# Optimization experiments

Measured on AMD Instinct MI355X. Metric: run time of the kernel, lower is better.

Reference implementation:

```python
import jax, jax.numpy as jnp
import numpy as np
from jax.scipy.linalg import solve_triangular

B, D, NL, NH, DH = 16, 768, 12, 12, 64
P, S, LP, NC = 10, 5, 5, 100
IMG, PATCH = 224, 16
NPTOK = (IMG // PATCH) ** 2  # 196 patches
DFF = 4 * D
LOG2PI = float(np.log(2.0 * np.pi))


def setup_inputs() -> dict:
    key = jax.random.key(0)
    ks = jax.random.split(key, 12)
    s = 0.02
    inp = {}
    inp['inputs'] = jax.random.normal(ks[0], (B, 3, IMG, IMG), jnp.float32)
    inp['patch_w'] = jax.random.normal(ks[1], (D, 3, PATCH, PATCH), jnp.float32) * s
    inp['patch_b'] = jnp.zeros((D,), jnp.float32)
    inp['cls_token'] = jax.random.normal(ks[2], (1, 1, D), jnp.float32) * s
    inp['pos_embed'] = jax.random.normal(ks[3], (1, NPTOK + 1, D), jnp.float32) * s
    inp['ln1_g'] = jnp.ones((NL, D), jnp.float32)
    inp['ln1_b'] = jnp.zeros((NL, D), jnp.float32)
    inp['qkv_w'] = jax.random.normal(ks[4], (NL, D, 3 * D), jnp.float32) * s
    inp['qkv_b'] = jnp.zeros((NL, 3 * D), jnp.float32)
    inp['proj_w'] = jax.random.normal(ks[5], (NL, D, D), jnp.float32) * s
    inp['proj_b'] = jnp.zeros((NL, D), jnp.float32)
    inp['ln2_g'] = jnp.ones((NL, D), jnp.float32)
    inp['ln2_b'] = jnp.zeros((NL, D), jnp.float32)
    inp['fc1_w'] = jax.random.normal(ks[6], (NL, D, DFF), jnp.float32) * s
    inp['fc1_b'] = jnp.zeros((NL, DFF), jnp.float32)
    inp['fc2_w'] = jax.random.normal(ks[7], (NL, DFF, D), jnp.float32) * s
    inp['fc2_b'] = jnp.zeros((NL, D), jnp.float32)
    inp['norm_g'] = jnp.ones((D,), jnp.float32)
    inp['norm_b'] = jnp.zeros((D,), jnp.float32)
    inp['head_w'] = jax.random.normal(ks[8], (D, NC), jnp.float32) * s
    inp['head_b'] = jnp.zeros((NC,), jnp.float32)
    inp['prompt'] = jax.random.normal(ks[9], (P, LP, D), jnp.float32)
    m = jax.random.normal(ks[10], (P, D), jnp.float32)
    inp['mean'] = m / jnp.linalg.norm(m, axis=-1, keepdims=True)
    # init in torch: ones + eye, repeated per pool component (positive definite)
    inp['variance'] = jnp.ones((P, D, D), jnp.float32) + jnp.eye(D, dtype=jnp.float32)[None]
    return inp


def _ln(x, g, b, eps=1e-6):
    m = x.mean(-1, keepdims=True)
    v = jnp.mean((x - m) ** 2, axis=-1, keepdims=True)
    return (x - m) * jax.lax.rsqrt(v + eps) * g + b


def _blocks(x, blk):
    def step(x, pl):
        g1, b1, qw, qb, pw, pb, g2, b2, f1w, f1b, f2w, f2b = pl
        Bn, N, _ = x.shape
        h = _ln(x, g1, b1)
        qkv = (h @ qw + qb).reshape(Bn, N, 3, NH, DH).transpose(2, 0, 3, 1, 4)
        q, k, v = qkv[0], qkv[1], qkv[2]  # [B,H,N,dh]
        att = jax.nn.softmax(jnp.einsum('bhqd,bhkd->bhqk', q, k) * (1.0 / np.sqrt(DH)), axis=-1)
        o = jnp.einsum('bhqk,bhkd->bhqd', att, v).transpose(0, 2, 1, 3).reshape(Bn, N, D)
        x = x + o @ pw + pb
        h = _ln(x, g2, b2)
        return x + jax.nn.gelu(h @ f1w + f1b) @ f2w + f2b, None
    x, _ = jax.lax.scan(step, x, blk)
    return x


def _mvn_logprob(q, mean, cov):
    # q: [B,D]; mean: [P,D]; cov: [P,D,D] -> [B,P]
    L = jnp.linalg.cholesky(cov)
    diff = q[:, None, :] - mean[None]  # [B,P,D]
    y = jax.vmap(lambda Lp, dp: solve_triangular(Lp, dp.T, lower=True), in_axes=(0, 1))(L, diff)  # [P,D,B]
    quad = jnp.sum(y * y, axis=1).T  # [B,P]
    logdet = 2.0 * jnp.sum(jnp.log(jnp.diagonal(L, axis1=-2, axis2=-1)), axis=-1)  # [P]
    return -0.5 * (D * LOG2PI + logdet[None, :] + quad)


def reference(inputs, patch_w, patch_b, cls_token, pos_embed, ln1_g, ln1_b, qkv_w, qkv_b,
              proj_w, proj_b, ln2_g, ln2_b, fc1_w, fc1_b, fc2_w, fc2_b, norm_g, norm_b,
              head_w, head_b, prompt, mean, variance):
    blk = (ln1_g, ln1_b, qkv_w, qkv_b, proj_w, proj_b, ln2_g, ln2_b, fc1_w, fc1_b, fc2_w, fc2_b)
    # patch embed: conv16x16 stride16 -> [B,196,D]
    img = jax.lax.conv_general_dilated(inputs, patch_w, (PATCH, PATCH), 'VALID',
                                       dimension_numbers=('NCHW', 'OIHW', 'NCHW'))
    img = img.reshape(B, D, NPTOK).transpose(0, 2, 1) + patch_b
    t = jnp.concatenate([jnp.broadcast_to(cls_token, (B, 1, D)), img], axis=1)
    x0 = t + pos_embed
    # query pass (no_grad in original)
    q = _ln(_blocks(x0, blk), norm_g, norm_b)[:, 0]  # [B,D]
    cov = jnp.abs(variance) + jnp.eye(D, dtype=variance.dtype)[None]
    logp = _mvn_logprob(q, mean, cov)  # [B,P]
    _, topk = jax.lax.top_k(logp, S)  # [B,S]
    prompts = prompt[topk].reshape(B, S * LP, D) + pos_embed[0, 0]
    # prompted pass: [cls(+pos), prompts, raw patch tokens]
    x = jnp.concatenate([x0[:, :1], prompts, img], axis=1)  # [B, 1+S*LP+196, D]
    x = _ln(_blocks(x, blk), norm_g, norm_b)
    x = x[:, 1:S * LP + 1].mean(axis=1)  # mean over prompt tokens
    return x @ head_w + head_b  # [B,NC]
```

## Files before the change

kernel.cpp:

```cpp
#include <hip/hip_runtime.h>
#include <stdint.h>
#include <math.h>


typedef _Float16 h16_t;
typedef _Float16 h8v __attribute__((ext_vector_type(8)));
typedef _Float16 h4v __attribute__((ext_vector_type(4)));
typedef float    f4v __attribute__((ext_vector_type(4)));

#define DEV static __device__ __forceinline__

DEV float wred64(float s) {
#pragma unroll
  for (int m = 1; m < 64; m <<= 1) s += __shfl_xor(s, m, 64);
  return s;
}
DEV float gelu_f(float x) {
  float u = 0.7978845608028654f * x * (1.0f + 0.044715f * x * x);
  u = fminf(fmaxf(u, -30.0f), 30.0f);
  float e = __expf(-2.0f * u);
  return 0.5f * x * (1.0f + (1.0f - e) / (1.0f + e));
}

#define GLD16(gp, lp) __builtin_amdgcn_global_load_lds( \
  (const __attribute__((address_space(1))) unsigned int*)(const void*)(gp), \
  (__attribute__((address_space(3))) unsigned int*)(void*)(lp), 16, 0, 0)

template <int R>
DEV void stgN(const h16_t* __restrict__ src, int row0, int rowmax, int ldk,
              char* ldsb, unsigned lbase, int tid) {
#pragma unroll
  for (int r = 0; r < R; r++) {
    unsigned P = ((unsigned)r << 13) + ((unsigned)tid << 4);
    unsigned Q = P ^ (((P >> 7) & 3u) << 4);
    int row = (int)(Q >> 6);
    int kb = (int)((Q & 63u) >> 1);
    int gr = row0 + row; gr = gr < rowmax ? gr : rowmax - 1;
    GLD16(src + (size_t)gr * ldk + kb,
          ldsb + lbase + (r << 13) + ((tid >> 6) << 10));
  }
}

#define FENCE() asm volatile("" ::: "memory")
#define RBAR() do { FENCE(); __builtin_amdgcn_s_barrier(); FENCE(); } while (0)
#define VMW(N) asm volatile("s_waitcnt vmcnt(" #N ")" ::: "memory")

DEV h8v frag_rd(const char* ldsb, unsigned rb, int row, int quad) {
  unsigned P = ((unsigned)row << 6) + ((unsigned)quad << 4);
  P ^= ((P >> 7) & 3u) << 4;
  return *(const h8v*)(ldsb + rb + P);
}

__global__ __launch_bounds__(512, 2) void hgemm_q(
    const h16_t* __restrict__ A, const h16_t* __restrict__ B,
    h16_t* __restrict__ C16, const float* __restrict__ bias,
    int M, int N, int K, int ldc16)
{
  __shared__ __align__(16) char ldsb[147456];
  int tid = threadIdx.x;
  int w = tid >> 6, lane = tid & 63;
  int wm = w >> 2, wn = w & 3;
  int fr = lane & 15, quad = lane >> 4;
  int m0 = blockIdx.x << 7, n0 = blockIdx.y << 8;

  f4v acc[4][4];
#pragma unroll
  for (int i2 = 0; i2 < 4; i2++)
#pragma unroll
    for (int j2 = 0; j2 < 4; j2++)
#pragma unroll
      for (int r2 = 0; r2 < 4; r2++) acc[i2][j2][r2] = 0.0f;

  int NT = K >> 6;

  auto stage = [&](int t, unsigned bb) {
    stgN<1>(A + (t << 6),      m0, M, K, ldsb, bb,           tid);
    stgN<1>(A + (t << 6) + 32, m0, M, K, ldsb, bb + 8192u,   tid);
    stgN<2>(B + (t << 6),      n0, N, K, ldsb, bb + 16384u,  tid);
    stgN<2>(B + (t << 6) + 32, n0, N, K, ldsb, bb + 32768u,  tid);
  };
  stage(0, 0u);
  stage(1, 49152u);
  VMW(6);
  __builtin_amdgcn_s_barrier();
  FENCE();

  unsigned cb = 0u, sb = 98304u;
  for (int i = 0; i < NT; i++) {
    int tS = (i + 2 < NT) ? i + 2 : NT - 1;
    stage(tS, sb);
    h8v af[2][4], bf[2][4];
#pragma unroll
    for (int kh = 0; kh < 2; kh++)
#pragma unroll
      for (int t = 0; t < 4; t++) {
        af[kh][t] = frag_rd(ldsb, cb + ((unsigned)kh << 13),
                            (wm << 6) + (t << 4) + fr, quad);
        bf[kh][t] = frag_rd(ldsb, cb + 16384u + ((unsigned)kh << 14),
                            (wn << 6) + (t << 4) + fr, quad);
      }
    __builtin_amdgcn_s_setprio(1);
#pragma unroll
    for (int kh = 0; kh < 2; kh++)
#pragma unroll
      for (int ti = 0; ti < 4; ti++)
#pragma unroll
        for (int tj = 0; tj < 4; tj++)
          acc[ti][tj] = __builtin_amdgcn_mfma_f32_16x16x32_f16(af[kh][ti], bf[kh][tj], acc[ti][tj], 0, 0, 0);
    __builtin_amdgcn_s_setprio(0);
    VMW(6);
    RBAR();
    cb = (cb == 98304u) ? 0u : cb + 49152u;
    sb = (sb == 98304u) ? 0u : sb + 49152u;
  }
  asm volatile("s_waitcnt vmcnt(0)" ::: "memory");

  int row0 = m0 + (wm << 6) + (quad << 2);
  int col0 = n0 + (wn << 6) + fr;
  float bv[4];
#pragma unroll
  for (int nj = 0; nj < 4; nj++) bv[nj] = bias[col0 + (nj << 4)];
#pragma unroll
  for (int mi = 0; mi < 4; mi++) {
#pragma unroll
    for (int rg = 0; rg < 4; rg++) {
      int row = row0 + (mi << 4) + rg;
      if (row < M) {
#pragma unroll
        for (int nj = 0; nj < 4; nj++) {
          float v = acc[mi][nj][rg] + bv[nj];
          C16[(size_t)row * ldc16 + col0 + (nj << 4)] = (h16_t)v;
        }
      }
    }
  }
}

__global__ __launch_bounds__(512, 2) void hgemm_f(
    const h16_t* __restrict__ A, const h16_t* __restrict__ B,
    h16_t* __restrict__ C16, const float* __restrict__ bias,
    int M, int N, int K, int ldc16)
{
  __shared__ __align__(16) char ldsb[98304];
  int tid = threadIdx.x;
  int w = tid >> 6, lane = tid & 63;
  int wm = w >> 2, wn = w & 3;
  int fr = lane & 15, quad = lane >> 4;
  int m0 = blockIdx.x << 8, n0 = blockIdx.y << 8;

  f4v acc[8][4];
#pragma unroll
  for (int i2 = 0; i2 < 8; i2++)
#pragma unroll
    for (int j2 = 0; j2 < 4; j2++)
#pragma unroll
      for (int r2 = 0; r2 < 4; r2++) acc[i2][j2][r2] = 0.0f;

  int NT = K >> 5;

  auto stage = [&](int t, unsigned bb) {
    stgN<2>(A + (t << 5), m0, M, K, ldsb, bb,          tid);
    stgN<2>(B + (t << 5), n0, N, K, ldsb, bb + 16384u, tid);
  };
  stage(0, 0u);
  stage(1, 32768u);
  VMW(4);
  __builtin_amdgcn_s_barrier();
  FENCE();

  unsigned cb = 0u, sb = 65536u;
  for (int i = 0; i < NT; i++) {
    int tS = (i + 2 < NT) ? i + 2 : NT - 1;
    stage(tS, sb);
    h8v af[8], bf[4];
#pragma unroll
    for (int t = 0; t < 8; t++)
      af[t] = frag_rd(ldsb, cb, (wm << 7) + (t << 4) + fr, quad);
#pragma unroll
    for (int t = 0; t < 4; t++)
      bf[t] = frag_rd(ldsb, cb + 16384u, (wn << 6) + (t << 4) + fr, quad);
    __builtin_amdgcn_s_setprio(1);
#pragma unroll
    for (int ti = 0; ti < 8; ti++)
#pragma unroll
      for (int tj = 0; tj < 4; tj++)
        acc[ti][tj] = __builtin_amdgcn_mfma_f32_16x16x32_f16(af[ti], bf[tj], acc[ti][tj], 0, 0, 0);
    __builtin_amdgcn_s_setprio(0);
    VMW(4);
    RBAR();
    cb = (cb == 65536u) ? 0u : cb + 32768u;
    sb = (sb == 65536u) ? 0u : sb + 32768u;
  }
  asm volatile("s_waitcnt vmcnt(0)" ::: "memory");

  int row0 = m0 + (wm << 7) + (quad << 2);
  int col0 = n0 + (wn << 6) + fr;
  float bv[4];
#pragma unroll
  for (int nj = 0; nj < 4; nj++) bv[nj] = bias[col0 + (nj << 4)];
#pragma unroll
  for (int mi = 0; mi < 8; mi++) {
#pragma unroll
    for (int rg = 0; rg < 4; rg++) {
      int row = row0 + (mi << 4) + rg;
      if (row < M) {
#pragma unroll
        for (int nj = 0; nj < 4; nj++) {
          float v = gelu_f(acc[mi][nj][rg] + bv[nj]);
          C16[(size_t)row * ldc16 + col0 + (nj << 4)] = (h16_t)v;
        }
      }
    }
  }
}

__global__ __launch_bounds__(512, 2) void hgemm_p(
    const h16_t* __restrict__ A, const h16_t* __restrict__ B,
    float* __restrict__ C32, const float* __restrict__ bias,
    int M, int N, int K, int ldc, int addC)
{
  __shared__ __align__(16) char ldsb[98304];
  int tid = threadIdx.x;
  int w = tid >> 6, lane = tid & 63;
  int wm = w >> 2, wn = w & 3;
  int fr = lane & 15, quad = lane >> 4;
  int m0 = blockIdx.x << 7, n0 = blockIdx.y << 7;

  f4v acc[4][2];
#pragma unroll
  for (int i2 = 0; i2 < 4; i2++)
#pragma unroll
    for (int j2 = 0; j2 < 2; j2++)
#pragma unroll
      for (int r2 = 0; r2 < 4; r2++) acc[i2][j2][r2] = 0.0f;

  int NT = K >> 6;

  auto stage = [&](int t, unsigned bb) {
    stgN<1>(A + (t << 6),      m0, M, K, ldsb, bb,           tid);
    stgN<1>(A + (t << 6) + 32, m0, M, K, ldsb, bb + 8192u,   tid);
    stgN<1>(B + (t << 6),      n0, N, K, ldsb, bb + 16384u,  tid);
    stgN<1>(B + (t << 6) + 32, n0, N, K, ldsb, bb + 24576u,  tid);
  };
  stage(0, 0u);
  stage(1, 32768u);
  VMW(4);
  __builtin_amdgcn_s_barrier();
  FENCE();

  unsigned cb = 0u, sb = 65536u;
  for (int i = 0; i < NT; i++) {
    int tS = (i + 2 < NT) ? i + 2 : NT - 1;
    stage(tS, sb);
    h8v af[2][4], bf[2][2];
#pragma unroll
    for (int kh = 0; kh < 2; kh++) {
#pragma unroll
      for (int t = 0; t < 4; t++)
        af[kh][t] = frag_rd(ldsb, cb + ((unsigned)kh << 13),
                            (wm << 6) + (t << 4) + fr, quad);
#pragma unroll
      for (int t = 0; t < 2; t++)
        bf[kh][t] = frag_rd(ldsb, cb + 16384u + ((unsigned)kh << 13),
                            (wn << 5) + (t << 4) + fr, quad);
    }
    __builtin_amdgcn_s_setprio(1);
#pragma unroll
    for (int kh = 0; kh < 2; kh++)
#pragma unroll
      for (int ti = 0; ti < 4; ti++)
#pragma unroll
        for (int tj = 0; tj < 2; tj++)
          acc[ti][tj] = __builtin_amdgcn_mfma_f32_16x16x32_f16(af[kh][ti], bf[kh][tj], acc[ti][tj], 0, 0, 0);
    __builtin_amdgcn_s_setprio(0);
    VMW(4);
    RBAR();
    cb = (cb == 65536u) ? 0u : cb + 32768u;
    sb = (sb == 65536u) ? 0u : sb + 32768u;
  }
  asm volatile("s_waitcnt vmcnt(0)" ::: "memory");

  int row0 = m0 + (wm << 6) + (quad << 2);
  int col0 = n0 + (wn << 5) + fr;
  float bv[2];
#pragma unroll
  for (int nj = 0; nj < 2; nj++) bv[nj] = bias[col0 + (nj << 4)];
#pragma unroll
  for (int mi = 0; mi < 4; mi++) {
#pragma unroll
    for (int rg = 0; rg < 4; rg++) {
      int row = row0 + (mi << 4) + rg;
      if (row < M) {
#pragma unroll
        for (int nj = 0; nj < 2; nj++) {
          size_t off = (size_t)row * ldc + col0 + (nj << 4);
          float v = acc[mi][nj][rg] + bv[nj];
          if (addC) v += C32[off];
          C32[off] = v;
        }
      }
    }
  }
}

__global__ __launch_bounds__(256) void flash_attn(
    const h16_t* __restrict__ qkv, h16_t* __restrict__ o, int N)
{
  int z = blockIdx.y;
  int b = z / 12, h = z - (z / 12) * 12;
  const h16_t* base = qkv + (size_t)b * N * 2304 + h * 64;
  int q0 = blockIdx.x << 6;
  int tid = threadIdx.x, w = tid >> 6, lane = tid & 63;
  int fr = lane & 15, fk = (lane >> 4) << 3;
  int quad = lane >> 4;

  __shared__ __align__(16) h16_t Qs[2][64 * 32];
  __shared__ __align__(16) h16_t Ks[2][64 * 32];
  __shared__ __align__(16) h16_t Ps[4][1024];
  __shared__ __align__(16) h16_t Vt[64 * 68];

#pragma unroll
  for (int s = 0; s < 2; s++) {
    int gq = q0 + (w << 4) + (lane >> 2); gq = gq < N ? gq : N - 1;
    GLD16(base + (size_t)gq * 2304 + (s << 5) + ((lane & 3) << 3), &Qs[s][(w << 4) << 5]);
  }
  __syncthreads();
  h8v af0 = *(const h8v*)&Qs[0][(((w << 4) + fr) << 5) + fk];
  h8v af1 = *(const h8v*)&Qs[1][(((w << 4) + fr) << 5) + fk];

  float mrow[4], lrow[4];
  f4v accO[4];
#pragma unroll
  for (int r = 0; r < 4; r++) { mrow[r] = -1e30f; lrow[r] = 0.0f; }
#pragma unroll
  for (int t = 0; t < 4; t++)
#pragma unroll
    for (int r = 0; r < 4; r++) accO[t][r] = 0.0f;

  int nj = (N + 63) >> 6;
  for (int jt = 0; jt < nj; jt++) {
    int j0 = jt << 6;
    __syncthreads();
#pragma unroll
    for (int s = 0; s < 2; s++) {
      int gj = j0 + (w << 4) + (lane >> 2); gj = gj < N ? gj : N - 1;
      GLD16(base + (size_t)gj * 2304 + 768 + (s << 5) + ((lane & 3) << 3), &Ks[s][(w << 4) << 5]);
    }
#pragma unroll
    for (int i = 0; i < 16; i++) {
      int j = (w << 4) + i;
      int gj = j0 + j; gj = gj < N ? gj : N - 1;
      Vt[lane * 68 + j] = base[(size_t)gj * 2304 + 1536 + lane];
    }
    __syncthreads();

    f4v s4[4];
#pragma unroll
    for (int t = 0; t < 4; t++) {
      h8v b0 = *(const h8v*)&Ks[0][(((t << 4) + fr) << 5) + fk];
      h8v b1 = *(const h8v*)&Ks[1][(((t << 4) + fr) << 5) + fk];
      f4v s; s[0] = s[1] = s[2] = s[3] = 0.0f;
      s = __builtin_amdgcn_mfma_f32_16x16x32_f16(af0, b0, s, 0, 0, 0);
      s = __builtin_amdgcn_mfma_f32_16x16x32_f16(af1, b1, s, 0, 0, 0);
      s4[t] = s;
    }
#pragma unroll
    for (int r = 0; r < 4; r++) {
      float tm = -1e30f;
#pragma unroll
      for (int t = 0; t < 4; t++) {
        float v = s4[t][r] * 0.125f;
        if (j0 + (t << 4) + fr >= N) v = -1e30f;
        s4[t][r] = v;
        tm = fmaxf(tm, v);
      }
#pragma unroll
      for (int m = 1; m < 16; m <<= 1) tm = fmaxf(tm, __shfl_xor(tm, m, 64));
      float mn = fmaxf(mrow[r], tm);
      float alpha = __expf(mrow[r] - mn);
      mrow[r] = mn;
      float rs = 0.0f;
#pragma unroll
      for (int t = 0; t < 4; t++) {
        float e = __expf(s4[t][r] - mn);
        s4[t][r] = e;
        rs += e;
      }
#pragma unroll
      for (int m = 1; m < 16; m <<= 1) rs += __shfl_xor(rs, m, 64);
      lrow[r] = lrow[r] * alpha + rs;
#pragma unroll
      for (int t = 0; t < 4; t++) accO[t][r] *= alpha;
#pragma unroll
      for (int t = 0; t < 4; t++)
        Ps[w][((t >> 1) << 9) + (((quad << 2) + r) << 5) + ((t & 1) << 4) + fr] = (h16_t)s4[t][r];
    }
#pragma unroll
    for (int s = 0; s < 2; s++) {
      h8v ap = *(const h8v*)&Ps[w][(s << 9) + (fr << 5) + fk];
#pragma unroll
      for (int t = 0; t < 4; t++) {
        int vidx = ((t << 4) + fr) * 68 + (s << 5) + fk;
        h4v v0 = *(const h4v*)&Vt[vidx];
        h4v v1 = *(const h4v*)&Vt[vidx + 4];
        h8v bv;
#pragma unroll
        for (int i = 0; i < 4; i++) { bv[i] = v0[i]; bv[i + 4] = v1[i]; }
        accO[t] = __builtin_amdgcn_mfma_f32_16x16x32_f16(ap, bv, accO[t], 0, 0, 0);
      }
    }
  }

#pragma unroll
  for (int r = 0; r < 4; r++) {
    int q = q0 + (w << 4) + (quad << 2) + r;
    if (q >= N) continue;
    float inv = 1.0f / lrow[r];
    h16_t* op = o + ((size_t)b * N + q) * 768 + h * 64 + fr;
#pragma unroll
    for (int t = 0; t < 4; t++) op[t << 4] = (h16_t)(accO[t][r] * inv);
  }
}

__global__ __launch_bounds__(256) void wcvt_t(const float* __restrict__ in,
                                              h16_t* __restrict__ o, int K, int N) {
  int z = blockIdx.z;
  in += (size_t)z * K * N;
  o  += (size_t)z * K * N;
  int n0 = blockIdx.x << 5, k0 = blockIdx.y << 5;
  __shared__ float t[32][33];
  int a = threadIdx.x >> 3, b4 = (threadIdx.x & 7) << 2;
  f4v v = *(const f4v*)(in + (size_t)(k0 + a) * N + n0 + b4);
  t[a][b4] = v[0]; t[a][b4 + 1] = v[1]; t[a][b4 + 2] = v[2]; t[a][b4 + 3] = v[3];
  __syncthreads();
  h4v h;
#pragma unroll
  for (int i = 0; i < 4; i++) h[i] = (h16_t)t[b4 + i][a];
  *(h4v*)(o + (size_t)(n0 + a) * K + k0 + b4) = h;
}

__global__ void cvt_flat(const float* __restrict__ in, h16_t* __restrict__ o, int n) {
  int i = blockIdx.x * 256 + threadIdx.x;
  if (i < n) o[i] = (h16_t)in[i];
}

__global__ void im2col_k(const float* __restrict__ in, h16_t* __restrict__ col) {
  int idx = blockIdx.x * 256 + threadIdx.x;
  if (idx >= 16 * 196 * 768) return;
  int k = idx % 768; int t = idx / 768; int p2 = t % 196; int b = t / 196;
  int c = k >> 8, ij = k & 255, i = ij >> 4, j = ij & 15;
  int py = p2 / 14, px = p2 % 14;
  col[idx] = (h16_t)in[(((size_t)b * 3 + c) * 224 + py * 16 + i) * 224 + px * 16 + j];
}

__global__ void build_x0_k(float* __restrict__ x, const float* __restrict__ img,
                           const float* __restrict__ cls, const float* __restrict__ pos) {
  int idx = blockIdx.x * 256 + threadIdx.x;
  if (idx >= 16 * 197 * 768) return;
  int d = idx % 768; int t = idx / 768; int n = t % 197; int b = t / 197;
  float v = (n == 0) ? cls[d] : img[((size_t)b * 196 + (n - 1)) * 768 + d];
  x[idx] = v + pos[n * 768 + d];
}

__global__ void build_x2_k(float* __restrict__ x, const float* __restrict__ img,
                           const float* __restrict__ cls, const float* __restrict__ pos,
                           const float* __restrict__ prompt, const int* __restrict__ tk) {
  int idx = blockIdx.x * 256 + threadIdx.x;
  if (idx >= 16 * 222 * 768) return;
  int d = idx % 768; int t = idx / 768; int n = t % 222; int b = t / 222;
  float v;
  if (n == 0) v = cls[d] + pos[d];
  else if (n < 26) {
    int s = (n - 1) / 5, li = (n - 1) % 5;
    v = prompt[((size_t)tk[b * 5 + s] * 5 + li) * 768 + d] + pos[d];
  } else {
    v = img[((size_t)b * 196 + (n - 26)) * 768 + d];
  }
  x[idx] = v;
}

__global__ void ln_rows(const float* __restrict__ in, h16_t* __restrict__ o16,
                        float* __restrict__ o32, const float* __restrict__ g,
                        const float* __restrict__ b, int rows, long istr, long ostr) {
  int gw = ((blockIdx.x << 8) + threadIdx.x) >> 6;
  int lane = threadIdx.x & 63;
  if (gw >= rows) return;
  const float* rp = in + (size_t)gw * istr;
  float v[12]; float s = 0;
#pragma unroll
  for (int i = 0; i < 12; i++) { v[i] = rp[lane + (i << 6)]; s += v[i]; }
  s = wred64(s);
  float mean = s * (1.0f / 768.0f);
  float s2 = 0;
#pragma unroll
  for (int i = 0; i < 12; i++) { float d = v[i] - mean; s2 += d * d; }
  s2 = wred64(s2);
  float rstd = rsqrtf(s2 * (1.0f / 768.0f) + 1e-6f);
#pragma unroll
  for (int i = 0; i < 12; i++) {
    int k = lane + (i << 6);
    float o = (v[i] - mean) * rstd * g[k] + b[k];
    if (o16) o16[(size_t)gw * ostr + k] = (h16_t)o;
    if (o32) o32[(size_t)gw * ostr + k] = o;
  }
}

__global__ void cov_init_k(const float* __restrict__ var, float* __restrict__ Lb) {
  size_t i = (size_t)blockIdx.x * 256 + threadIdx.x;
  if (i >= (size_t)10 * 589824) return;
  int ij = (int)(i % 589824);
  int r = ij / 768, c = ij - r * 768;
  Lb[i] = fabsf(var[i]) + ((r == c) ? 1.0f : 0.0f);
}

__global__ __launch_bounds__(256) void sgemm_nt_chol(float* __restrict__ Lb, int jb) {
  int p = blockIdx.z;
  float* base = Lb + (size_t)p * 589824;
  const float* A = base + (size_t)jb * 768;
  const float* Bp = A;
  float* C = base + (size_t)jb * 768 + jb;
  int m0 = blockIdx.x << 6;
  __shared__ float As[16][64];
  __shared__ float Bs[16][64];
  int tid = threadIdx.x;
  int am = tid & 63, ak = (tid >> 6) << 2;
  int tm = (tid >> 4) << 2, tn = (tid & 15) << 2;
  float acc[4][4] = {};
  for (int k0 = 0; k0 < jb; k0 += 16) {
    f4v va = *(const f4v*)(A + (size_t)(m0 + am) * 768 + k0 + ak);
    f4v vb = *(const f4v*)(Bp + (size_t)am * 768 + k0 + ak);
#pragma unroll
    for (int i = 0; i < 4; i++) { As[ak + i][am] = va[i]; Bs[ak + i][am] = vb[i]; }
    __syncthreads();
#pragma unroll
    for (int kk = 0; kk < 16; kk++) {
      f4v a = *(const f4v*)&As[kk][tm];
      f4v b = *(const f4v*)&Bs[kk][tn];
#pragma unroll
      for (int i = 0; i < 4; i++)
#pragma unroll
        for (int j = 0; j < 4; j++) acc[i][j] += a[i] * b[j];
    }
    __syncthreads();
  }
#pragma unroll
  for (int i = 0; i < 4; i++)
#pragma unroll
    for (int j = 0; j < 4; j++)
      C[(size_t)(m0 + tm + i) * 768 + tn + j] -= acc[i][j];
}

template <int CB>
DEV void chol_sub(float (&row)[64], int r, bool actv, float* Bl, float* Dg, float* Dinv) {
  if constexpr (CB > 0) {
    if (actv && r >= CB && r < CB + 16) {
      int c = r - CB;
#pragma unroll
      for (int k = 0; k < CB; k++) Bl[k * 16 + c] = row[k];
    }
    __syncthreads();
    if (actv && r >= CB) {
#pragma unroll
      for (int k = 0; k < CB; k++) {
        float a = row[k];
#pragma unroll
        for (int c = 0; c < 16; c++) row[CB + c] -= a * Bl[k * 16 + c];
      }
    }
  }
  __syncthreads();
  if (r >= CB && r < CB + 16) {
    int c = r - CB;
#pragma unroll
    for (int j = 0; j < 16; j++) {
      float dv = __shfl(row[CB + j], CB + j, 64);
      float ds = sqrtf(dv);
      float di = 1.0f / ds;
      if (c == j) row[CB + j] = ds;
      else if (c > j) row[CB + j] *= di;
#pragma unroll
      for (int c2 = j + 1; c2 < 16; c2++) {
        float lc2 = __shfl(row[CB + j], CB + c2, 64);
        if (c >= c2) row[CB + c2] -= row[CB + j] * lc2;
      }
    }
#pragma unroll
    for (int j = 0; j < 16; j++) Dg[c * 16 + j] = row[CB + j];
    Dinv[c] = 1.0f / row[CB + c];
  }
  __syncthreads();
  if (actv && r >= CB + 16) {
#pragma unroll
    for (int c2 = 0; c2 < 16; c2++) {
      float v = row[CB + c2];
#pragma unroll
      for (int k = 0; k < c2; k++) v -= row[CB + k] * Dg[c2 * 16 + k];
      row[CB + c2] = v * Dinv[c2];
    }
  }
  __syncthreads();
}

__global__ __launch_bounds__(768) void chol_panel(float* __restrict__ Lb, int jb) {
  int p = blockIdx.x;
  float* L = Lb + (size_t)p * 589824;
  int R = 768 - jb;
  int r = threadIdx.x;
  bool actv = r < R;
  __shared__ float Bl[48 * 16];
  __shared__ float Dg[256];
  __shared__ float Dinv[16];
  float row[64];
  float* my = L + (size_t)(jb + r) * 768 + jb;
  if (actv) {
#pragma unroll
    for (int i = 0; i < 16; i++) {
      f4v v = *(const f4v*)(my + 4 * i);
      row[4 * i] = v[0]; row[4 * i + 1] = v[1]; row[4 * i + 2] = v[2]; row[4 * i + 3] = v[3];
    }
  }
  chol_sub<0>(row, r, actv, Bl, Dg, Dinv);
  chol_sub<16>(row, r, actv, Bl, Dg, Dinv);
  chol_sub<32>(row, r, actv, Bl, Dg, Dinv);
  chol_sub<48>(row, r, actv, Bl, Dg, Dinv);
  if (actv) {
#pragma unroll
    for (int i = 0; i < 16; i++) {
      f4v v; v[0] = row[4 * i]; v[1] = row[4 * i + 1]; v[2] = row[4 * i + 2]; v[3] = row[4 * i + 3];
      *(f4v*)(my + 4 * i) = v;
    }
  }
}

__global__ __launch_bounds__(256) void ltrans_k(const float* __restrict__ Lb,
                                                float* __restrict__ Ut,
                                                float* __restrict__ dg) {
  int p = blockIdx.z;
  const float* L = Lb + (size_t)p * 589824;
  float* U = Ut + (size_t)p * 589824;
  int r0 = blockIdx.x << 5, c0 = blockIdx.y << 5;
  __shared__ float t[32][33];
  int a = threadIdx.x >> 3, b4 = (threadIdx.x & 7) << 2;
  f4v v = *(const f4v*)(L + (size_t)(r0 + a) * 768 + c0 + b4);
  t[a][b4] = v[0]; t[a][b4 + 1] = v[1]; t[a][b4 + 2] = v[2]; t[a][b4 + 3] = v[3];
  __syncthreads();
  int k = c0 + a;
  f4v ov;
#pragma unroll
  for (int i = 0; i < 4; i++) {
    int j = r0 + b4 + i;
    float val = t[b4 + i][a];
    ov[i] = (j > k) ? val : 0.0f;
    if (j == k) dg[p * 768 + k] = val;
  }
  *(f4v*)(U + (size_t)k * 768 + r0 + b4) = ov;
}

__global__ __launch_bounds__(64) void trsm2(const float* __restrict__ Ut,
                                            const float* __restrict__ dg,
                                            const float* __restrict__ q,
                                            const float* __restrict__ mean,
                                            float* __restrict__ logp) {
  int gw = blockIdx.x;
  int p = gw >> 4, b = gw & 15;
  const float* U = Ut + (size_t)p * 589824;
  int lane = threadIdx.x;

  float y[12], dinv[12];
  float lacc = 0.0f;
#pragma unroll
  for (int m = 0; m < 12; m++) {
    int i = lane + (m << 6);
    y[m] = q[b * 768 + i] - mean[p * 768 + i];
    float d = dg[p * 768 + i];
    dinv[m] = 1.0f / d;
    lacc += __logf(d);
  }

  float u[8][12];
#pragma unroll
  for (int d0 = 0; d0 < 8; d0++)
#pragma unroll
    for (int mm = 0; mm < 12; mm++)
      u[d0][mm] = U[(size_t)d0 * 768 + lane + (mm << 6)];

#pragma unroll
  for (int m = 0; m < 12; m++) {
    for (int kb = 0; kb < 64; kb += 8) {
#pragma unroll
      for (int kd = 0; kd < 8; kd++) {
        int k = (m << 6) + kb + kd;
        float yo = __shfl(y[m], kb + kd, 64);
        float di = __shfl(dinv[m], kb + kd, 64);
        float yk = yo * di;
        if (lane == kb + kd) y[m] = yk;
        float un[12];
        bool pf = (k + 8) < 768;
        const float* rp = U + (size_t)(k + 8) * 768 + lane;
#pragma unroll
        for (int mm = 0; mm < 12; mm++) un[mm] = pf ? rp[mm << 6] : 0.0f;
#pragma unroll
        for (int mm = 0; mm < 12; mm++) y[mm] -= u[kd][mm] * yk;
#pragma unroll
        for (int mm = 0; mm < 12; mm++) u[kd][mm] = un[mm];
      }
    }
  }

  float quad = 0.0f;
#pragma unroll
  for (int m = 0; m < 12; m++) quad += y[m] * y[m];
  quad = wred64(quad);
  lacc = wred64(lacc);
  if (lane == 0)
    logp[b * 10 + p] = -0.5f * (768.0f * 1.8378770664093453f + 2.0f * lacc + quad);
}

__global__ void topk_k(const float* __restrict__ logp, int* __restrict__ tk) {
  int b = threadIdx.x;
  if (b >= 16) return;
  float v[10];
#pragma unroll
  for (int p = 0; p < 10; p++) v[p] = logp[b * 10 + p];
#pragma unroll
  for (int s = 0; s < 5; s++) {
    int bi = 0; float bv = v[0];
#pragma unroll
    for (int p = 1; p < 10; p++) if (v[p] > bv) { bv = v[p]; bi = p; }
    tk[b * 5 + s] = bi;
    v[bi] = -3.0e38f;
  }
}

DEV float blocksum256(float s, float* red) {
  s = wred64(s);
  __syncthreads();
  if ((threadIdx.x & 63) == 0) red[threadIdx.x >> 6] = s;
  __syncthreads();
  return red[0] + red[1] + red[2] + red[3];
}

__global__ __launch_bounds__(256) void final_head(const float* __restrict__ x,
                                                  const float* __restrict__ g,
                                                  const float* __restrict__ b,
                                                  const float* __restrict__ hw,
                                                  const float* __restrict__ hb,
                                                  float* __restrict__ out) {
  int bb = blockIdx.x, tid = threadIdx.x;
  __shared__ float xm[768];
  __shared__ float red[4];
  float a0 = 0, a1 = 0, a2 = 0;
  for (int j = 1; j <= 25; j++) {
    const float* rp = x + ((size_t)bb * 222 + j) * 768;
    float v0 = rp[tid], v1 = rp[tid + 256], v2 = rp[tid + 512];
    float s = blocksum256(v0 + v1 + v2, red);
    float mean = s * (1.0f / 768.0f);
    float d0 = v0 - mean, d1 = v1 - mean, d2 = v2 - mean;
    float s2 = blocksum256(d0 * d0 + d1 * d1 + d2 * d2, red);
    float rstd = rsqrtf(s2 * (1.0f / 768.0f) + 1e-6f);
    a0 += d0 * rstd * g[tid] + b[tid];
    a1 += d1 * rstd * g[tid + 256] + b[tid + 256];
    a2 += d2 * rstd * g[tid + 512] + b[tid + 512];
  }
  xm[tid] = a0 * (1.0f / 25.0f);
  xm[tid + 256] = a1 * (1.0f / 25.0f);
  xm[tid + 512] = a2 * (1.0f / 25.0f);
  __syncthreads();
  if (tid < 100) {
    float s = hb[tid];
    for (int d = 0; d < 768; d++) s += xm[d] * hw[d * 100 + tid];
    out[bb * 100 + tid] = s;
  }
}

extern "C" void kernel_launch(void* const* d_in, const int* in_sizes, int n_in,
                              void* d_out, int out_size, void* d_ws, size_t ws_size,
                              hipStream_t stream) {
  (void)in_sizes; (void)n_in; (void)out_size; (void)ws_size;
  const float* inp     = (const float*)d_in[0];
  const float* patchw  = (const float*)d_in[1];
  const float* patchb  = (const float*)d_in[2];
  const float* cls     = (const float*)d_in[3];
  const float* pos     = (const float*)d_in[4];
  const float* ln1g    = (const float*)d_in[5];
  const float* ln1b    = (const float*)d_in[6];
  const float* qkvw    = (const float*)d_in[7];
  const float* qkvb    = (const float*)d_in[8];
  const float* projw   = (const float*)d_in[9];
  const float* projb   = (const float*)d_in[10];
  const float* ln2g    = (const float*)d_in[11];
  const float* ln2b    = (const float*)d_in[12];
  const float* fc1w    = (const float*)d_in[13];
  const float* fc1b    = (const float*)d_in[14];
  const float* fc2w    = (const float*)d_in[15];
  const float* fc2b    = (const float*)d_in[16];
  const float* normg   = (const float*)d_in[17];
  const float* normb   = (const float*)d_in[18];
  const float* headw   = (const float*)d_in[19];
  const float* headb   = (const float*)d_in[20];
  const float* prompt  = (const float*)d_in[21];
  const float* meanp   = (const float*)d_in[22];
  const float* var     = (const float*)d_in[23];
  float* out = (float*)d_out;

  char* ws = (char*)d_ws;
  size_t cur = 0;
  auto alloc = [&](size_t bytes) { size_t r = cur; cur += (bytes + 255) & ~(size_t)255; return r; };
  float* x    = (float*)(ws + alloc((size_t)3552 * 768 * 4));
  float* img  = (float*)(ws + alloc((size_t)3136 * 768 * 4));
  float* qb   = (float*)(ws + alloc((size_t)16 * 768 * 4));
  float* logp = (float*)(ws + alloc(1024));
  int*   tk   = (int*)(ws + alloc(1024));
  float* dg   = (float*)(ws + alloc((size_t)10 * 768 * 4));
  h16_t* h16   = (h16_t*)(ws + alloc((size_t)3552 * 768 * 2));
  size_t qkv_off = alloc((size_t)3552 * 2304 * 2);
  h16_t* qkv16 = (h16_t*)(ws + qkv_off);
  size_t g_off = alloc((size_t)3552 * 3072 * 2);
  h16_t* g16   = (h16_t*)(ws + g_off);
  float* Lbuf  = (float*)(ws + alloc((size_t)10 * 589824 * 4));
  h16_t* wq16  = (h16_t*)(ws + alloc((size_t)12 * 2304 * 768 * 2));
  h16_t* wp16  = (h16_t*)(ws + alloc((size_t)12 * 768 * 768 * 2));
  h16_t* w116  = (h16_t*)(ws + alloc((size_t)12 * 3072 * 768 * 2));
  h16_t* w216  = (h16_t*)(ws + alloc((size_t)12 * 768 * 3072 * 2));
  h16_t* wpt16 = (h16_t*)(ws + alloc((size_t)768 * 768 * 2));
  h16_t* col16 = (h16_t*)(ws + g_off);
  float* Ut    = (float*)(ws + qkv_off);

  wcvt_t<<<dim3(72, 24, 12), 256, 0, stream>>>(qkvw, wq16, 768, 2304);
  wcvt_t<<<dim3(24, 24, 12), 256, 0, stream>>>(projw, wp16, 768, 768);
  wcvt_t<<<dim3(96, 24, 12), 256, 0, stream>>>(fc1w, w116, 768, 3072);
  wcvt_t<<<dim3(24, 96, 12), 256, 0, stream>>>(fc2w, w216, 3072, 768);
  cvt_flat<<<2304, 256, 0, stream>>>(patchw, wpt16, 589824);

  im2col_k<<<9408, 256, 0, stream>>>(inp, col16);
  hgemm_p<<<dim3(25, 6), 512, 0, stream>>>(col16, wpt16, img, patchb,
      3136, 768, 768, 768, 0);
  build_x0_k<<<9456, 256, 0, stream>>>(x, img, cls, pos);

  auto pass = [&](int Ntok) {
    int M = 16 * Ntok;
    int Mt1 = (M + 127) / 128;
    int Mt8 = (M + 255) / 256;
    int Qt = (Ntok + 63) / 64;
    for (int l = 0; l < 12; l++) {
      ln_rows<<<(M + 3) / 4, 256, 0, stream>>>(x, h16, nullptr, ln1g + l * 768, ln1b + l * 768, M, 768, 768);
      hgemm_q<<<dim3(Mt1, 9), 512, 0, stream>>>(h16, wq16 + (size_t)l * 2304 * 768, qkv16,
          qkvb + l * 2304, M, 2304, 768, 2304);
      flash_attn<<<dim3(Qt, 192), 256, 0, stream>>>(qkv16, h16, Ntok);
      hgemm_p<<<dim3(Mt1, 6), 512, 0, stream>>>(h16, wp16 + (size_t)l * 768 * 768, x,
          projb + l * 768, M, 768, 768, 768, 1);
      ln_rows<<<(M + 3) / 4, 256, 0, stream>>>(x, h16, nullptr, ln2g + l * 768, ln2b + l * 768, M, 768, 768);
      hgemm_f<<<dim3(Mt8, 12), 512, 0, stream>>>(h16, w116 + (size_t)l * 3072 * 768, g16,
          fc1b + l * 3072, M, 3072, 768, 3072);
      hgemm_p<<<dim3(Mt1, 6), 512, 0, stream>>>(g16, w216 + (size_t)l * 768 * 3072, x,
          fc2b + l * 768, M, 768, 3072, 768, 1);
    }
  };

  pass(197);
  ln_rows<<<4, 256, 0, stream>>>(x, nullptr, qb, normg, normb, 16, (long)197 * 768, 768);

  cov_init_k<<<23040, 256, 0, stream>>>(var, Lbuf);
  for (int m = 0; m < 12; m++) {
    int jb = 64 * m;
    if (m) sgemm_nt_chol<<<dim3((768 - jb) / 64, 1, 10), 256, 0, stream>>>(Lbuf, jb);
    chol_panel<<<10, 768, 0, stream>>>(Lbuf, jb);
  }
  ltrans_k<<<dim3(24, 24, 10), 256, 0, stream>>>(Lbuf, Ut, dg);
  trsm2<<<160, 64, 0, stream>>>(Ut, dg, qb, meanp, logp);
  topk_k<<<1, 64, 0, stream>>>(logp, tk);

  build_x2_k<<<10656, 256, 0, stream>>>(x, img, cls, pos, prompt, tk);
  pass(222);
  final_head<<<16, 256, 0, stream>>>(x, normg, normb, headw, headb, out);
}
```

Baseline: 5.333 ms.

## Switch blocked Cholesky from left-looking panel to right-looking diag/trsm/syrk steps

Replaces the left-looking blocked Cholesky (a GEMM update followed by a single 768-thread panel kernel per matrix) with a right-looking scheme. Each step factors the 64x64 diagonal block in one wave, solves the off-diagonal panel with one thread per row, and applies a lower-triangular trailing SYRK update over many 64x64 tiles. The aim is more parallel blocks per step than the old 10-block panel kernel, which did serial sub-block work. In exchange there are more kernel launches, the trailing submatrix is re-read and re-written at every step, and the diagonal factorization runs in only 64 threads per matrix.

```diff
diff --git a/kernel.cpp b/kernel.cpp
--- a/kernel.cpp
+++ b/kernel.cpp
@@ -513,21 +513,93 @@
   Lb[i] = fabsf(var[i]) + ((r == c) ? 1.0f : 0.0f);
 }
 
-__global__ __launch_bounds__(256) void sgemm_nt_chol(float* __restrict__ Lb, int jb) {
+__global__ __launch_bounds__(64) void chol_diag(float* __restrict__ Lb, int jb) {
+  int p = blockIdx.x;
+  float* base = Lb + (size_t)p * 589824 + (size_t)jb * 768 + jb;
+  int r = threadIdx.x;
+  float* rp = base + (size_t)r * 768;
+  float a[64];
+#pragma unroll
+  for (int i = 0; i < 16; i++) {
+    f4v v = *(const f4v*)(rp + 4 * i);
+    a[4 * i] = v[0]; a[4 * i + 1] = v[1]; a[4 * i + 2] = v[2]; a[4 * i + 3] = v[3];
+  }
+#pragma unroll
+  for (int j = 0; j < 64; j++) {
+    float dv = __shfl(a[j], j, 64);
+    float ds = sqrtf(dv);
+    float di = 1.0f / ds;
+    if (r == j) a[j] = ds;
+    else if (r > j) a[j] *= di;
+    float lrj = a[j];
+#pragma unroll
+    for (int c = j + 1; c < 64; c++) {
+      float lcj = __shfl(a[j], c, 64);
+      if (r >= c) a[c] -= lrj * lcj;
+    }
+  }
+#pragma unroll
+  for (int i = 0; i < 16; i++) {
+    f4v v;
+    v[0] = a[4 * i]; v[1] = a[4 * i + 1]; v[2] = a[4 * i + 2]; v[3] = a[4 * i + 3];
+    *(f4v*)(rp + 4 * i) = v;
+  }
+}
+
+__global__ __launch_bounds__(256) void trsm_off(float* __restrict__ Lb, int jb, int R) {
+  int p = blockIdx.y;
+  float* base = Lb + (size_t)p * 589824;
+  __shared__ float L11[64][64];
+  int tid = threadIdx.x;
+  {
+    int rr = tid >> 2, cc = (tid & 3) << 4;
+    const float* sp = base + (size_t)(jb + rr) * 768 + jb + cc;
+#pragma unroll
+    for (int i = 0; i < 4; i++)
+      *(f4v*)&L11[rr][cc + 4 * i] = *(const f4v*)(sp + 4 * i);
+  }
+  __syncthreads();
+  int r = blockIdx.x * 256 + tid;
+  if (r >= R) return;
+  float* rp = base + (size_t)(jb + 64 + r) * 768 + jb;
+  float x[64];
+#pragma unroll
+  for (int i = 0; i < 16; i++) {
+    f4v v = *(const f4v*)(rp + 4 * i);
+    x[4 * i] = v[0]; x[4 * i + 1] = v[1]; x[4 * i + 2] = v[2]; x[4 * i + 3] = v[3];
+  }
+#pragma unroll
+  for (int c = 0; c < 64; c++) {
+    float s = x[c];
+#pragma unroll
+    for (int k = 0; k < c; k++) s -= x[k] * L11[c][k];
+    x[c] = s * (1.0f / L11[c][c]);
+  }
+#pragma unroll
+  for (int i = 0; i < 16; i++) {
+    f4v v;
+    v[0] = x[4 * i]; v[1] = x[4 * i + 1]; v[2] = x[4 * i + 2]; v[3] = x[4 * i + 3];
+    *(f4v*)(rp + 4 * i) = v;
+  }
+}
+
+__global__ __launch_bounds__(256) void syrk_upd(float* __restrict__ Lb, int jb) {
+  int bi = blockIdx.x, bj = blockIdx.y;
+  if (bj > bi) return;
   int p = blockIdx.z;
   float* base = Lb + (size_t)p * 589824;
-  const float* A = base + (size_t)jb * 768;
-  const float* Bp = A;
-  float* C = base + (size_t)jb * 768 + jb;
-  int m0 = blockIdx.x << 6;
+  int i0 = jb + 64 + (bi << 6), j0 = jb + 64 + (bj << 6);
+  const float* A = base + (size_t)i0 * 768 + jb;
+  const float* Bp = base + (size_t)j0 * 768 + jb;
+  float* C = base + (size_t)i0 * 768 + j0;
   __shared__ float As[16][64];
   __shared__ float Bs[16][64];
   int tid = threadIdx.x;
   int am = tid & 63, ak = (tid >> 6) << 2;
   int tm = (tid >> 4) << 2, tn = (tid & 15) << 2;
   float acc[4][4] = {};
-  for (int k0 = 0; k0 < jb; k0 += 16) {
-    f4v va = *(const f4v*)(A + (size_t)(m0 + am) * 768 + k0 + ak);
+  for (int k0 = 0; k0 < 64; k0 += 16) {
+    f4v va = *(const f4v*)(A + (size_t)am * 768 + k0 + ak);
     f4v vb = *(const f4v*)(Bp + (size_t)am * 768 + k0 + ak);
 #pragma unroll
     for (int i = 0; i < 4; i++) { As[ak + i][am] = va[i]; Bs[ak + i][am] = vb[i]; }
@@ -547,89 +619,7 @@
   for (int i = 0; i < 4; i++)
 #pragma unroll
     for (int j = 0; j < 4; j++)
-      C[(size_t)(m0 + tm + i) * 768 + tn + j] -= acc[i][j];
-}
-
-template <int CB>
-DEV void chol_sub(float (&row)[64], int r, bool actv, float* Bl, float* Dg, float* Dinv) {
-  if constexpr (CB > 0) {
-    if (actv && r >= CB && r < CB + 16) {
-      int c = r - CB;
-#pragma unroll
-      for (int k = 0; k < CB; k++) Bl[k * 16 + c] = row[k];
-    }
-    __syncthreads();
-    if (actv && r >= CB) {
-#pragma unroll
-      for (int k = 0; k < CB; k++) {
-        float a = row[k];
-#pragma unroll
-        for (int c = 0; c < 16; c++) row[CB + c] -= a * Bl[k * 16 + c];
-      }
-    }
-  }
-  __syncthreads();
-  if (r >= CB && r < CB + 16) {
-    int c = r - CB;
-#pragma unroll
-    for (int j = 0; j < 16; j++) {
-      float dv = __shfl(row[CB + j], CB + j, 64);
-      float ds = sqrtf(dv);
-      float di = 1.0f / ds;
-      if (c == j) row[CB + j] = ds;
-      else if (c > j) row[CB + j] *= di;
-#pragma unroll
-      for (int c2 = j + 1; c2 < 16; c2++) {
-        float lc2 = __shfl(row[CB + j], CB + c2, 64);
-        if (c >= c2) row[CB + c2] -= row[CB + j] * lc2;
-      }
-    }
-#pragma unroll
-    for (int j = 0; j < 16; j++) Dg[c * 16 + j] = row[CB + j];
-    Dinv[c] = 1.0f / row[CB + c];
-  }
-  __syncthreads();
-  if (actv && r >= CB + 16) {
-#pragma unroll
-    for (int c2 = 0; c2 < 16; c2++) {
-      float v = row[CB + c2];
-#pragma unroll
-      for (int k = 0; k < c2; k++) v -= row[CB + k] * Dg[c2 * 16 + k];
-      row[CB + c2] = v * Dinv[c2];
-    }
-  }
-  __syncthreads();
-}
-
-__global__ __launch_bounds__(768) void chol_panel(float* __restrict__ Lb, int jb) {
-  int p = blockIdx.x;
-  float* L = Lb + (size_t)p * 589824;
-  int R = 768 - jb;
-  int r = threadIdx.x;
-  bool actv = r < R;
-  __shared__ float Bl[48 * 16];
-  __shared__ float Dg[256];
-  __shared__ float Dinv[16];
-  float row[64];
-  float* my = L + (size_t)(jb + r) * 768 + jb;
-  if (actv) {
-#pragma unroll
-    for (int i = 0; i < 16; i++) {
-      f4v v = *(const f4v*)(my + 4 * i);
-      row[4 * i] = v[0]; row[4 * i + 1] = v[1]; row[4 * i + 2] = v[2]; row[4 * i + 3] = v[3];
-    }
-  }
-  chol_sub<0>(row, r, actv, Bl, Dg, Dinv);
-  chol_sub<16>(row, r, actv, Bl, Dg, Dinv);
-  chol_sub<32>(row, r, actv, Bl, Dg, Dinv);
-  chol_sub<48>(row, r, actv, Bl, Dg, Dinv);
-  if (actv) {
-#pragma unroll
-    for (int i = 0; i < 16; i++) {
-      f4v v; v[0] = row[4 * i]; v[1] = row[4 * i + 1]; v[2] = row[4 * i + 2]; v[3] = row[4 * i + 3];
-      *(f4v*)(my + 4 * i) = v;
-    }
-  }
+      C[(size_t)(tm + i) * 768 + tn + j] -= acc[i][j];
 }
 
 __global__ __launch_bounds__(256) void ltrans_k(const float* __restrict__ Lb,
@@ -863,8 +853,12 @@
   cov_init_k<<<23040, 256, 0, stream>>>(var, Lbuf);
   for (int m = 0; m < 12; m++) {
     int jb = 64 * m;
-    if (m) sgemm_nt_chol<<<dim3((768 - jb) / 64, 1, 10), 256, 0, stream>>>(Lbuf, jb);
-    chol_panel<<<10, 768, 0, stream>>>(Lbuf, jb);
+    chol_diag<<<10, 64, 0, stream>>>(Lbuf, jb);
+    int R = 704 - jb;
+    if (R > 0) {
+      trsm_off<<<dim3((R + 255) / 256, 10), 256, 0, stream>>>(Lbuf, jb, R);
+      syrk_upd<<<dim3(R >> 6, R >> 6, 10), 256, 0, stream>>>(Lbuf, jb);
+    }
   }
   ltrans_k<<<dim3(24, 24, 10), 256, 0, stream>>>(Lbuf, Ut, dg);
   trsm2<<<160, 64, 0, stream>>>(Ut, dg, qb, meanp, logp);
```

New measurement: 5.998 ms. 12.5% more time.
